# Kernel tuning notes

Measured on AMD Instinct MI355X. Metric: run time of the kernel, lower is better.

## Reference

```python
import jax, jax.numpy as jnp
import numpy as np

TOL_CONTACT = 0.01  # contact tolerance from signed_dis


def _knn_pair(ref_pts, ref_nrm, q_pts, k):
    """Signed distance from each query point to the surface of one other object.

    ref_pts/ref_nrm: [Nr,3] reference object points (in plane frame) and normals.
    q_pts: [Nq,3] query object points (in plane frame). Returns [Nq].
    """
    # brute-force squared distances [Nq, Nr] (same math as tra.nearest_neighbor)
    sq = (jnp.sum(q_pts * q_pts, -1)[:, None]
          - 2.0 * (q_pts @ ref_pts.T)
          + jnp.sum(ref_pts * ref_pts, -1)[None, :])
    negd, idx = jax.lax.top_k(-sq, k)                  # k nearest per query: [Nq,k]
    dist = jnp.sqrt(jnp.maximum(-negd, 0.0))           # euclidean distances
    near = ref_pts[idx]                                # [Nq,k,3] gathered surface pts
    near_n = ref_nrm[idx]                              # [Nq,k,3] gathered normals
    grad = near - q_pts[:, None, :]
    grad = grad / jnp.linalg.norm(grad, axis=-1, keepdims=True)
    insides = jnp.sum(near_n * grad, axis=-1) > 0      # einsum('okij,okij->oki')
    inside = jnp.sum(insides, axis=-1) > k * 0.8       # majority vote over k
    # nearest-neighbor distance, sign-flipped when inside
    return jnp.where(inside, -dist[:, 0], dist[:, 0])


def reference(points, est_T, plane_T, k):
    M, N, _ = points.shape
    # transform object points into plane frame
    T = jnp.linalg.inv(plane_T)[None] @ est_T          # [M,4,4]
    xyz = points[..., :3]
    nrm = points[..., 3:6]
    pts_pl = jnp.einsum('mij,mnj->mni', T[:, :3, :3], xyz) + T[:, None, :3, 3]
    sd_plane = pts_pl[..., 2]                          # plane signed distance [M,N]

    # signed distance of object b's points to every other object o: pair[b,o,:]
    pair = jax.vmap(
        lambda q: jax.vmap(lambda rp, rn: _knn_pair(rp, rn, q, k))(pts_pl, nrm)
    )(pts_pl)                                          # [M,M,N]
    big = jnp.asarray(jnp.finfo(pair.dtype).max, pair.dtype)
    pair = jnp.where(jnp.eye(M, dtype=bool)[:, :, None], big, pair)
    sd_obj = jnp.min(pair, axis=1)                     # min over other objects [M,N]

    signed_distance = jnp.minimum(sd_plane, sd_obj)
    intersects = signed_distance < -TOL_CONTACT
    return signed_distance, intersects


def setup_inputs() -> dict:
    key = jax.random.key(0)
    kp, kn, kt, kpl = jax.random.split(key, 4)
    M, N = 4, 3072
    # objects offset from each other so pairwise nearest distances are > 0
    xyz = jax.random.normal(kp, (M, N, 3), jnp.float32) * 0.05 \
        + jnp.arange(M, dtype=jnp.float32)[:, None, None] * 0.3
    nrm = jax.random.normal(kn, (M, N, 3), jnp.float32)
    nrm = nrm / jnp.linalg.norm(nrm, axis=-1, keepdims=True)
    points = jnp.concatenate([xyz, nrm], axis=-1)      # [M,N,6]

    def rigid(k_, n):
        q, _ = jnp.linalg.qr(jax.random.normal(k_, (n, 3, 3), jnp.float32))
        t = jax.random.normal(jax.random.fold_in(k_, 7), (n, 3), jnp.float32) * 0.1
        T = jnp.zeros((n, 4, 4), jnp.float32)
        T = T.at[:, :3, :3].set(q).at[:, :3, 3].set(t).at[:, 3, 3].set(1.0)
        return T

    est_T = rigid(kt, M)        # per-object estimated transforms [M,4,4]
    plane_T = rigid(kpl, 1)[0]  # plane transform [4,4]
    return {"points": points, "est_T": est_T, "plane_T": plane_T, "k": 10}
```

## Files before the change

### kernel.cpp

```cpp
#include <hip/hip_runtime.h>
#include <math.h>

#define M_OBJ 4
#define N_PTS 3072
#define K_NN  10
#define NSLOT (M_OBJ - 1)
#define QPB   64
#define SEG   4
#define SEGN  (N_PTS / SEG)
#define NCHUNK (SEGN / 64)
#define WSTRIDE 16
#define NWARM (SEGN / WSTRIDE)
#define IDBITS 12
#define IDMASK ((1u << IDBITS) - 1u)

__device__ inline void make_T(const float* __restrict__ E,
                              const float* __restrict__ P,
                              float T[3][4]) {
    float Pi[3][4];
#pragma unroll
    for (int i = 0; i < 3; ++i) {
#pragma unroll
        for (int j = 0; j < 3; ++j) Pi[i][j] = P[j * 4 + i];
        Pi[i][3] = -(P[0 * 4 + i] * P[3] + P[1 * 4 + i] * P[7] + P[2 * 4 + i] * P[11]);
    }
#pragma unroll
    for (int i = 0; i < 3; ++i) {
#pragma unroll
        for (int j = 0; j < 4; ++j) {
            float acc = (j == 3) ? Pi[i][3] : 0.0f;
#pragma unroll
            for (int kk = 0; kk < 3; ++kk) acc += Pi[i][kk] * E[kk * 4 + j];
            T[i][j] = acc;
        }
    }
}

__device__ __forceinline__ void insertv(float v, float bs[K_NN]) {
#pragma unroll
    for (int i = 0; i < K_NN - 1; ++i)
        bs[i] = __builtin_amdgcn_fmed3f(v, bs[i], bs[i + 1]);
    bs[K_NN - 1] = fmaxf(v, bs[K_NN - 1]);
}

__device__ __forceinline__ float score4(const float4 p, float qx, float qy, float qz) {
    return fmaf(p.x, qx, fmaf(p.y, qy, fmaf(p.z, qz, -p.w)));
}

__global__ __launch_bounds__(256, 3) void pair_kernel(
        const float* __restrict__ points,
        const float* __restrict__ estT,
        const float* __restrict__ planeT,
        float* __restrict__ pair_sd) {
    __shared__ float4 sref[N_PTS];
    __shared__ float  mbuf[128 * K_NN];

    const int pidx  = blockIdx.x;
    const int q     = pidx / NSLOT;
    const int rs    = pidx % NSLOT;
    const int r     = rs + (rs >= q ? 1 : 0);
    const int tid   = threadIdx.x;
    const int seg   = tid >> 6;
    const int qlane = tid & 63;

    float Tq[3][4], Tr[3][4];
    make_T(estT + q * 16, planeT, Tq);
    make_T(estT + r * 16, planeT, Tr);

    for (int j = tid; j < N_PTS; j += 256) {
        const float* p = points + (size_t)(r * N_PTS + j) * 6;
        float2 xy = *(const float2*)p;
        float  z  = p[2];
        float px = Tr[0][0] * xy.x + Tr[0][1] * xy.y + Tr[0][2] * z + Tr[0][3];
        float py = Tr[1][0] * xy.x + Tr[1][1] * xy.y + Tr[1][2] * z + Tr[1][3];
        float pz = Tr[2][0] * xy.x + Tr[2][1] * xy.y + Tr[2][2] * z + Tr[2][3];
        float w  = 0.5f * (px * px + py * py + pz * pz);
        sref[j] = make_float4(px, py, pz, w);
    }
    __syncthreads();

    const int nq = blockIdx.y * QPB + qlane;
    const float* qp = points + (size_t)(q * N_PTS + nq) * 6;
    float2 qxy = *(const float2*)qp;
    float  qzz = qp[2];
    const float qx = Tq[0][0] * qxy.x + Tq[0][1] * qxy.y + Tq[0][2] * qzz + Tq[0][3];
    const float qy = Tq[1][0] * qxy.x + Tq[1][1] * qxy.y + Tq[1][2] * qzz + Tq[1][3];
    const float qz = Tq[2][0] * qxy.x + Tq[2][1] * qxy.y + Tq[2][2] * qzz + Tq[2][3];
    const float qq = qx * qx + qy * qy + qz * qz;

    auto pack = [&](int id) -> float {
        float s = score4(sref[id], qx, qy, qz);
        return __uint_as_float((__float_as_uint(s) & ~IDMASK) | (unsigned)id);
    };

    float bs[K_NN];
#pragma unroll
    for (int i = 0; i < K_NN; ++i) bs[i] = -3.4e38f;

    const int j0 = seg * SEGN;

#pragma unroll 4
    for (int t = 0; t < NWARM; ++t)
        insertv(pack(j0 + t * WSTRIDE), bs);

    for (int c = 0; c < NCHUNK; ++c) {
        const int jj = j0 + c * 64;
        const float b0 = bs[0];
        const float gate = fmaf(-fabsf(b0), 1.0e-3f, b0) - 1e-30f;
        unsigned w0 = 0u, w1 = 0u;
#pragma unroll
        for (int b = 0; b < 32; ++b) {
            float s = score4(sref[jj + b], qx, qy, qz);
            w0 |= (s > gate) ? (1u << b) : 0u;
        }
#pragma unroll
        for (int b = 0; b < 32; ++b) {
            float s = score4(sref[jj + 32 + b], qx, qy, qz);
            w1 |= (s > gate) ? (1u << b) : 0u;
        }
        w0 &= ~0x00010001u;
        w1 &= ~0x00010001u;

        while (__any((w0 | w1) != 0u)) {
            if (w0) {
                const int b = __builtin_ctz(w0); w0 &= w0 - 1u;
                insertv(pack(jj + b), bs);
            }
            if (w1) {
                const int b = __builtin_ctz(w1); w1 &= w1 - 1u;
                insertv(pack(jj + 32 + b), bs);
            }
        }
    }

    __syncthreads();
    if (seg >= 2) {
        const int slot = tid - 128;
#pragma unroll
        for (int i = 0; i < K_NN; ++i) mbuf[slot * K_NN + i] = bs[i];
    }
    __syncthreads();
    if (seg < 2) {
        const int src = (seg * 64 + qlane) * K_NN;
#pragma unroll
        for (int i = 0; i < K_NN; ++i) insertv(mbuf[src + i], bs);
    }
    __syncthreads();
    if (seg == 1) {
#pragma unroll
        for (int i = 0; i < K_NN; ++i) mbuf[qlane * K_NN + i] = bs[i];
    }
    __syncthreads();
    if (seg == 0) {
        const int src = qlane * K_NN;
#pragma unroll
        for (int i = 0; i < K_NN; ++i) insertv(mbuf[src + i], bs);

        const float* nrm_base = points + (size_t)r * N_PTS * 6 + 3;
        int votes = 0;
        float s_best = -3.4e38f;
#pragma unroll
        for (int i = 0; i < K_NN; ++i) {
            const int id = (int)(__float_as_uint(bs[i]) & IDMASK);
            float4 p = sref[id];
            float s = score4(p, qx, qy, qz);
            if (i == K_NN - 1) s_best = s;
            const float* nb = nrm_base + (size_t)id * 6;
            float gx = p.x - qx, gy = p.y - qy, gz = p.z - qz;
            votes += (fmaf(nb[0], gx, fmaf(nb[1], gy, nb[2] * gz)) > 0.0f) ? 1 : 0;
        }

        float sq = fmaxf(fmaf(-2.0f, s_best, qq), 0.0f);
        float d0 = sqrtf(sq);
        float sd = (votes > 8) ? -d0 : d0;
        pair_sd[((size_t)q * NSLOT + rs) * N_PTS + nq] = sd;
    }
}

__global__ __launch_bounds__(256) void reduce_kernel(
        const float* __restrict__ points,
        const float* __restrict__ estT,
        const float* __restrict__ planeT,
        const float* __restrict__ pair_sd,
        float* __restrict__ out) {
    int i = blockIdx.x * blockDim.x + threadIdx.x;
    if (i >= M_OBJ * N_PTS) return;
    int m = i / N_PTS, n = i % N_PTS;

    float T[3][4];
    make_T(estT + m * 16, planeT, T);
    const float* p = points + (size_t)i * 6;
    float zpl = T[2][0] * p[0] + T[2][1] * p[1] + T[2][2] * p[2] + T[2][3];

    float sd = zpl;
#pragma unroll
    for (int rs = 0; rs < NSLOT; ++rs)
        sd = fminf(sd, pair_sd[((size_t)m * NSLOT + rs) * N_PTS + n]);

    out[i] = sd;
    out[M_OBJ * N_PTS + i] = (sd < -0.01f) ? 1.0f : 0.0f;
}

extern "C" void kernel_launch(void* const* d_in, const int* in_sizes, int n_in,
                              void* d_out, int out_size, void* d_ws, size_t ws_size,
                              hipStream_t stream) {
    const float* points = (const float*)d_in[0];
    const float* estT   = (const float*)d_in[1];
    const float* planeT = (const float*)d_in[2];

    float* pair_sd = (float*)d_ws;

    dim3 gridB(M_OBJ * NSLOT, N_PTS / QPB);
    pair_kernel<<<gridB, 256, 0, stream>>>(points, estT, planeT, pair_sd);

    int total = M_OBJ * N_PTS;
    reduce_kernel<<<(total + 255) / 256, 256, 0, stream>>>(points, estT, planeT,
                                                           pair_sd, (float*)d_out);
}
```

Measured before the change: 119.7 us.

## Process three queries per thread to reuse shared reference loads

Each thread now tracks top-k lists for three query points, sharing each shared-memory reference float4 load across three score computations. The grid's query dimension shrinks threefold and the launch bound drops to two blocks per CU to accommodate the extra registers. This reduces LDS read traffic and the redundant per-block reference staging, but lowers the number of blocks and serialises the three candidate-insertion loops per thread.

```diff
diff --git a/kernel.cpp b/kernel.cpp
--- a/kernel.cpp
+++ b/kernel.cpp
@@ -5,14 +5,13 @@
 #define N_PTS 3072
 #define K_NN  10
 #define NSLOT (M_OBJ - 1)
-#define QPB   64
-#define SEG   4
-#define SEGN  (N_PTS / SEG)
+#define QSL   3
+#define QPB   (64 * QSL)
+#define NQCH  (N_PTS / QPB)
+#define SEGN  (N_PTS / 4)
 #define NCHUNK (SEGN / 64)
-#define WSTRIDE 16
-#define NWARM (SEGN / WSTRIDE)
-#define IDBITS 12
-#define IDMASK ((1u << IDBITS) - 1u)
+#define NWARM (SEGN / 16)
+#define IDMASK 0xFFFu
 
 __device__ inline void make_T(const float* __restrict__ E,
                               const float* __restrict__ P,
@@ -47,15 +46,21 @@
     return fmaf(p.x, qx, fmaf(p.y, qy, fmaf(p.z, qz, -p.w)));
 }
 
-__global__ __launch_bounds__(256, 3) void pair_kernel(
+#define PACKQ(P, LID, QX, QY, QZ) \
+    __uint_as_float((__float_as_uint(score4((P), (QX), (QY), (QZ))) & ~IDMASK) | (unsigned)(LID))
+
+#define GATE_OF(B0) (fmaf(-fabsf(B0), 1.0e-3f, (B0)) - 1e-30f)
+
+__global__ __launch_bounds__(256, 2) void pair_kernel(
         const float* __restrict__ points,
         const float* __restrict__ estT,
         const float* __restrict__ planeT,
         float* __restrict__ pair_sd) {
     __shared__ float4 sref[N_PTS];
-    __shared__ float  mbuf[128 * K_NN];
+    __shared__ float  mbuf[128 * QSL * K_NN];
 
     const int pidx  = blockIdx.x;
+    const int qc    = blockIdx.y;
     const int q     = pidx / NSLOT;
     const int rs    = pidx % NSLOT;
     const int r     = rs + (rs >= q ? 1 : 0);
@@ -74,62 +79,87 @@
         float px = Tr[0][0] * xy.x + Tr[0][1] * xy.y + Tr[0][2] * z + Tr[0][3];
         float py = Tr[1][0] * xy.x + Tr[1][1] * xy.y + Tr[1][2] * z + Tr[1][3];
         float pz = Tr[2][0] * xy.x + Tr[2][1] * xy.y + Tr[2][2] * z + Tr[2][3];
-        float w  = 0.5f * (px * px + py * py + pz * pz);
-        sref[j] = make_float4(px, py, pz, w);
-    }
-    __syncthreads();
-
-    const int nq = blockIdx.y * QPB + qlane;
-    const float* qp = points + (size_t)(q * N_PTS + nq) * 6;
-    float2 qxy = *(const float2*)qp;
-    float  qzz = qp[2];
-    const float qx = Tq[0][0] * qxy.x + Tq[0][1] * qxy.y + Tq[0][2] * qzz + Tq[0][3];
-    const float qy = Tq[1][0] * qxy.x + Tq[1][1] * qxy.y + Tq[1][2] * qzz + Tq[1][3];
-    const float qz = Tq[2][0] * qxy.x + Tq[2][1] * qxy.y + Tq[2][2] * qzz + Tq[2][3];
-    const float qq = qx * qx + qy * qy + qz * qz;
-
-    auto pack = [&](int id) -> float {
-        float s = score4(sref[id], qx, qy, qz);
-        return __uint_as_float((__float_as_uint(s) & ~IDMASK) | (unsigned)id);
-    };
-
-    float bs[K_NN];
-#pragma unroll
-    for (int i = 0; i < K_NN; ++i) bs[i] = -3.4e38f;
+        sref[j] = make_float4(px, py, pz, 0.5f * (px * px + py * py + pz * pz));
+    }
+    __syncthreads();
+
+    const int nqA = qc * QPB + 0 * 64 + qlane;
+    const int nqB = qc * QPB + 1 * 64 + qlane;
+    const int nqC = qc * QPB + 2 * 64 + qlane;
+    const float* qpA = points + (size_t)(q * N_PTS + nqA) * 6;
+    const float* qpB = points + (size_t)(q * N_PTS + nqB) * 6;
+    const float* qpC = points + (size_t)(q * N_PTS + nqC) * 6;
+    float2 axy = *(const float2*)qpA; float az = qpA[2];
+    float2 bxy = *(const float2*)qpB; float bz = qpB[2];
+    float2 cxy = *(const float2*)qpC; float cz = qpC[2];
+    const float qxA = Tq[0][0]*axy.x + Tq[0][1]*axy.y + Tq[0][2]*az + Tq[0][3];
+    const float qyA = Tq[1][0]*axy.x + Tq[1][1]*axy.y + Tq[1][2]*az + Tq[1][3];
+    const float qzA = Tq[2][0]*axy.x + Tq[2][1]*axy.y + Tq[2][2]*az + Tq[2][3];
+    const float qxB = Tq[0][0]*bxy.x + Tq[0][1]*bxy.y + Tq[0][2]*bz + Tq[0][3];
+    const float qyB = Tq[1][0]*bxy.x + Tq[1][1]*bxy.y + Tq[1][2]*bz + Tq[1][3];
+    const float qzB = Tq[2][0]*bxy.x + Tq[2][1]*bxy.y + Tq[2][2]*bz + Tq[2][3];
+    const float qxC = Tq[0][0]*cxy.x + Tq[0][1]*cxy.y + Tq[0][2]*cz + Tq[0][3];
+    const float qyC = Tq[1][0]*cxy.x + Tq[1][1]*cxy.y + Tq[1][2]*cz + Tq[1][3];
+    const float qzC = Tq[2][0]*cxy.x + Tq[2][1]*cxy.y + Tq[2][2]*cz + Tq[2][3];
+    const float qqA = qxA*qxA + qyA*qyA + qzA*qzA;
+    const float qqB = qxB*qxB + qyB*qyB + qzB*qzB;
+    const float qqC = qxC*qxC + qyC*qyC + qzC*qzC;
+
+    float bsA[K_NN], bsB[K_NN], bsC[K_NN];
+#pragma unroll
+    for (int i = 0; i < K_NN; ++i) { bsA[i] = -3.4e38f; bsB[i] = -3.4e38f; bsC[i] = -3.4e38f; }
 
     const int j0 = seg * SEGN;
 
-#pragma unroll 4
-    for (int t = 0; t < NWARM; ++t)
-        insertv(pack(j0 + t * WSTRIDE), bs);
+    for (int k = 0; k < NWARM; ++k) {
+        const int lid = j0 + k * 16;
+        const float4 p = sref[lid];
+        insertv(PACKQ(p, lid, qxA, qyA, qzA), bsA);
+        insertv(PACKQ(p, lid, qxB, qyB, qzB), bsB);
+        insertv(PACKQ(p, lid, qxC, qyC, qzC), bsC);
+    }
 
     for (int c = 0; c < NCHUNK; ++c) {
         const int jj = j0 + c * 64;
-        const float b0 = bs[0];
-        const float gate = fmaf(-fabsf(b0), 1.0e-3f, b0) - 1e-30f;
-        unsigned w0 = 0u, w1 = 0u;
+        const float gA = GATE_OF(bsA[0]);
+        const float gB = GATE_OF(bsB[0]);
+        const float gC = GATE_OF(bsC[0]);
+        unsigned mA0 = 0u, mA1 = 0u, mB0 = 0u, mB1 = 0u, mC0 = 0u, mC1 = 0u;
 #pragma unroll
         for (int b = 0; b < 32; ++b) {
-            float s = score4(sref[jj + b], qx, qy, qz);
-            w0 |= (s > gate) ? (1u << b) : 0u;
+            const float4 p = sref[jj + b];
+            mA0 |= (score4(p, qxA, qyA, qzA) > gA) ? (1u << b) : 0u;
+            mB0 |= (score4(p, qxB, qyB, qzB) > gB) ? (1u << b) : 0u;
+            mC0 |= (score4(p, qxC, qyC, qzC) > gC) ? (1u << b) : 0u;
         }
 #pragma unroll
         for (int b = 0; b < 32; ++b) {
-            float s = score4(sref[jj + 32 + b], qx, qy, qz);
-            w1 |= (s > gate) ? (1u << b) : 0u;
-        }
-        w0 &= ~0x00010001u;
-        w1 &= ~0x00010001u;
-
-        while (__any((w0 | w1) != 0u)) {
-            if (w0) {
-                const int b = __builtin_ctz(w0); w0 &= w0 - 1u;
-                insertv(pack(jj + b), bs);
-            }
-            if (w1) {
-                const int b = __builtin_ctz(w1); w1 &= w1 - 1u;
-                insertv(pack(jj + 32 + b), bs);
-            }
+            const float4 p = sref[jj + 32 + b];
+            mA1 |= (score4(p, qxA, qyA, qzA) > gA) ? (1u << b) : 0u;
+            mB1 |= (score4(p, qxB, qyB, qzB) > gB) ? (1u << b) : 0u;
+            mC1 |= (score4(p, qxC, qyC, qzC) > gC) ? (1u << b) : 0u;
+        }
+        mA0 &= ~0x00010001u; mA1 &= ~0x00010001u;
+        mB0 &= ~0x00010001u; mB1 &= ~0x00010001u;
+        mC0 &= ~0x00010001u; mC1 &= ~0x00010001u;
+
+        while (__any((mA0 | mA1) != 0u)) {
+            if (mA0) { const int b = __builtin_ctz(mA0); mA0 &= mA0 - 1u;
+                const int lid = jj + b;      insertv(PACKQ(sref[lid], lid, qxA, qyA, qzA), bsA); }
+            if (mA1) { const int b = __builtin_ctz(mA1); mA1 &= mA1 - 1u;
+                const int lid = jj + 32 + b; insertv(PACKQ(sref[lid], lid, qxA, qyA, qzA), bsA); }
+        }
+        while (__any((mB0 | mB1) != 0u)) {
+            if (mB0) { const int b = __builtin_ctz(mB0); mB0 &= mB0 - 1u;
+                const int lid = jj + b;      insertv(PACKQ(sref[lid], lid, qxB, qyB, qzB), bsB); }
+            if (mB1) { const int b = __builtin_ctz(mB1); mB1 &= mB1 - 1u;
+                const int lid = jj + 32 + b; insertv(PACKQ(sref[lid], lid, qxB, qyB, qzB), bsB); }
+        }
+        while (__any((mC0 | mC1) != 0u)) {
+            if (mC0) { const int b = __builtin_ctz(mC0); mC0 &= mC0 - 1u;
+                const int lid = jj + b;      insertv(PACKQ(sref[lid], lid, qxC, qyC, qzC), bsC); }
+            if (mC1) { const int b = __builtin_ctz(mC1); mC1 &= mC1 - 1u;
+                const int lid = jj + 32 + b; insertv(PACKQ(sref[lid], lid, qxC, qyC, qzC), bsC); }
         }
     }
 
@@ -137,43 +167,84 @@
     if (seg >= 2) {
         const int slot = tid - 128;
 #pragma unroll
-        for (int i = 0; i < K_NN; ++i) mbuf[slot * K_NN + i] = bs[i];
+        for (int i = 0; i < K_NN; ++i) {
+            mbuf[(slot * QSL + 0) * K_NN + i] = bsA[i];
+            mbuf[(slot * QSL + 1) * K_NN + i] = bsB[i];
+            mbuf[(slot * QSL + 2) * K_NN + i] = bsC[i];
+        }
     }
     __syncthreads();
     if (seg < 2) {
-        const int src = (seg * 64 + qlane) * K_NN;
-#pragma unroll
-        for (int i = 0; i < K_NN; ++i) insertv(mbuf[src + i], bs);
+        const int src = seg * 64 + qlane;
+#pragma unroll
+        for (int i = 0; i < K_NN; ++i) {
+            insertv(mbuf[(src * QSL + 0) * K_NN + i], bsA);
+            insertv(mbuf[(src * QSL + 1) * K_NN + i], bsB);
+            insertv(mbuf[(src * QSL + 2) * K_NN + i], bsC);
+        }
     }
     __syncthreads();
     if (seg == 1) {
 #pragma unroll
-        for (int i = 0; i < K_NN; ++i) mbuf[qlane * K_NN + i] = bs[i];
+        for (int i = 0; i < K_NN; ++i) {
+            mbuf[(qlane * QSL + 0) * K_NN + i] = bsA[i];
+            mbuf[(qlane * QSL + 1) * K_NN + i] = bsB[i];
+            mbuf[(qlane * QSL + 2) * K_NN + i] = bsC[i];
+        }
     }
     __syncthreads();
     if (seg == 0) {
-        const int src = qlane * K_NN;
-#pragma unroll
-        for (int i = 0; i < K_NN; ++i) insertv(mbuf[src + i], bs);
+#pragma unroll
+        for (int i = 0; i < K_NN; ++i) {
+            insertv(mbuf[(qlane * QSL + 0) * K_NN + i], bsA);
+            insertv(mbuf[(qlane * QSL + 1) * K_NN + i], bsB);
+            insertv(mbuf[(qlane * QSL + 2) * K_NN + i], bsC);
+        }
 
         const float* nrm_base = points + (size_t)r * N_PTS * 6 + 3;
-        int votes = 0;
-        float s_best = -3.4e38f;
-#pragma unroll
-        for (int i = 0; i < K_NN; ++i) {
-            const int id = (int)(__float_as_uint(bs[i]) & IDMASK);
-            float4 p = sref[id];
-            float s = score4(p, qx, qy, qz);
-            if (i == K_NN - 1) s_best = s;
-            const float* nb = nrm_base + (size_t)id * 6;
-            float gx = p.x - qx, gy = p.y - qy, gz = p.z - qz;
-            votes += (fmaf(nb[0], gx, fmaf(nb[1], gy, nb[2] * gz)) > 0.0f) ? 1 : 0;
-        }
-
-        float sq = fmaxf(fmaf(-2.0f, s_best, qq), 0.0f);
-        float d0 = sqrtf(sq);
-        float sd = (votes > 8) ? -d0 : d0;
-        pair_sd[((size_t)q * NSLOT + rs) * N_PTS + nq] = sd;
+
+        {
+            int votes = 0; float s_best = -3.4e38f;
+#pragma unroll
+            for (int i = 0; i < K_NN; ++i) {
+                const int id = (int)(__float_as_uint(bsA[i]) & IDMASK);
+                const float4 p = sref[id];
+                const float s = score4(p, qxA, qyA, qzA);
+                if (i == K_NN - 1) s_best = s;
+                const float* nb = nrm_base + (size_t)id * 6;
+                votes += (fmaf(nb[0], p.x-qxA, fmaf(nb[1], p.y-qyA, nb[2]*(p.z-qzA))) > 0.0f) ? 1 : 0;
+            }
+            const float d0 = sqrtf(fmaxf(fmaf(-2.0f, s_best, qqA), 0.0f));
+            pair_sd[((size_t)q * NSLOT + rs) * N_PTS + nqA] = (votes > 8) ? -d0 : d0;
+        }
+        {
+            int votes = 0; float s_best = -3.4e38f;
+#pragma unroll
+            for (int i = 0; i < K_NN; ++i) {
+                const int id = (int)(__float_as_uint(bsB[i]) & IDMASK);
+                const float4 p = sref[id];
+                const float s = score4(p, qxB, qyB, qzB);
+                if (i == K_NN - 1) s_best = s;
+                const float* nb = nrm_base + (size_t)id * 6;
+                votes += (fmaf(nb[0], p.x-qxB, fmaf(nb[1], p.y-qyB, nb[2]*(p.z-qzB))) > 0.0f) ? 1 : 0;
+            }
+            const float d0 = sqrtf(fmaxf(fmaf(-2.0f, s_best, qqB), 0.0f));
+            pair_sd[((size_t)q * NSLOT + rs) * N_PTS + nqB] = (votes > 8) ? -d0 : d0;
+        }
+        {
+            int votes = 0; float s_best = -3.4e38f;
+#pragma unroll
+            for (int i = 0; i < K_NN; ++i) {
+                const int id = (int)(__float_as_uint(bsC[i]) & IDMASK);
+                const float4 p = sref[id];
+                const float s = score4(p, qxC, qyC, qzC);
+                if (i == K_NN - 1) s_best = s;
+                const float* nb = nrm_base + (size_t)id * 6;
+                votes += (fmaf(nb[0], p.x-qxC, fmaf(nb[1], p.y-qyC, nb[2]*(p.z-qzC))) > 0.0f) ? 1 : 0;
+            }
+            const float d0 = sqrtf(fmaxf(fmaf(-2.0f, s_best, qqC), 0.0f));
+            pair_sd[((size_t)q * NSLOT + rs) * N_PTS + nqC] = (votes > 8) ? -d0 : d0;
+        }
     }
 }
 
@@ -190,9 +261,7 @@
     float T[3][4];
     make_T(estT + m * 16, planeT, T);
     const float* p = points + (size_t)i * 6;
-    float zpl = T[2][0] * p[0] + T[2][1] * p[1] + T[2][2] * p[2] + T[2][3];
-
-    float sd = zpl;
+    float sd = T[2][0]*p[0] + T[2][1]*p[1] + T[2][2]*p[2] + T[2][3];
 #pragma unroll
     for (int rs = 0; rs < NSLOT; ++rs)
         sd = fminf(sd, pair_sd[((size_t)m * NSLOT + rs) * N_PTS + n]);
@@ -210,7 +279,7 @@
 
     float* pair_sd = (float*)d_ws;
 
-    dim3 gridB(M_OBJ * NSLOT, N_PTS / QPB);
+    dim3 gridB(M_OBJ * NSLOT, NQCH);
     pair_kernel<<<gridB, 256, 0, stream>>>(points, estT, planeT, pair_sd);
 
     int total = M_OBJ * N_PTS;
```

After: 348.2 us. 191% more time.

## Share top-k pruning threshold across segment warps and widen scan chunks

Applied to the files above, without the earlier changes.

After the strided warm-up pass, each of the four segment warps writes its current k-th-best score to shared memory. Every warp then gates candidates against the maximum of those four values, and refreshes it once mid-scan. This prunes more insertion work than using only the warp's own running k-th best. The scan loop also tests 128 reference points per iteration with four bitmasks instead of 64, which amortises the divergent insertion loop. The cost is extra block barriers and a larger register footprint under the 3-blocks-per-SM launch bound.

```diff
diff --git a/kernel.cpp b/kernel.cpp
--- a/kernel.cpp
+++ b/kernel.cpp
@@ -6,13 +6,10 @@
 #define K_NN  10
 #define NSLOT (M_OBJ - 1)
 #define QPB   64
-#define SEG   4
-#define SEGN  (N_PTS / SEG)
+#define SEGN  (N_PTS / 4)
 #define NCHUNK (SEGN / 64)
-#define WSTRIDE 16
-#define NWARM (SEGN / WSTRIDE)
-#define IDBITS 12
-#define IDMASK ((1u << IDBITS) - 1u)
+#define NWARM (SEGN / 16)
+#define IDMASK 0xFFFu
 
 __device__ inline void make_T(const float* __restrict__ E,
                               const float* __restrict__ P,
@@ -46,6 +43,10 @@
 __device__ __forceinline__ float score4(const float4 p, float qx, float qy, float qz) {
     return fmaf(p.x, qx, fmaf(p.y, qy, fmaf(p.z, qz, -p.w)));
 }
+
+#define PACKQ(P, LID, QX, QY, QZ) \
+    __uint_as_float((__float_as_uint(score4((P), (QX), (QY), (QZ))) & ~IDMASK) | (unsigned)(LID))
+#define GATE_OF(B0) (fmaf(-fabsf(B0), 1.0e-3f, (B0)) - 1e-30f)
 
 __global__ __launch_bounds__(256, 3) void pair_kernel(
         const float* __restrict__ points,
@@ -74,8 +75,7 @@
         float px = Tr[0][0] * xy.x + Tr[0][1] * xy.y + Tr[0][2] * z + Tr[0][3];
         float py = Tr[1][0] * xy.x + Tr[1][1] * xy.y + Tr[1][2] * z + Tr[1][3];
         float pz = Tr[2][0] * xy.x + Tr[2][1] * xy.y + Tr[2][2] * z + Tr[2][3];
-        float w  = 0.5f * (px * px + py * py + pz * pz);
-        sref[j] = make_float4(px, py, pz, w);
+        sref[j] = make_float4(px, py, pz, 0.5f * (px * px + py * py + pz * pz));
     }
     __syncthreads();
 
@@ -83,15 +83,10 @@
     const float* qp = points + (size_t)(q * N_PTS + nq) * 6;
     float2 qxy = *(const float2*)qp;
     float  qzz = qp[2];
-    const float qx = Tq[0][0] * qxy.x + Tq[0][1] * qxy.y + Tq[0][2] * qzz + Tq[0][3];
-    const float qy = Tq[1][0] * qxy.x + Tq[1][1] * qxy.y + Tq[1][2] * qzz + Tq[1][3];
-    const float qz = Tq[2][0] * qxy.x + Tq[2][1] * qxy.y + Tq[2][2] * qzz + Tq[2][3];
-    const float qq = qx * qx + qy * qy + qz * qz;
-
-    auto pack = [&](int id) -> float {
-        float s = score4(sref[id], qx, qy, qz);
-        return __uint_as_float((__float_as_uint(s) & ~IDMASK) | (unsigned)id);
-    };
+    const float qx = Tq[0][0]*qxy.x + Tq[0][1]*qxy.y + Tq[0][2]*qzz + Tq[0][3];
+    const float qy = Tq[1][0]*qxy.x + Tq[1][1]*qxy.y + Tq[1][2]*qzz + Tq[1][3];
+    const float qz = Tq[2][0]*qxy.x + Tq[2][1]*qxy.y + Tq[2][2]*qzz + Tq[2][3];
+    const float qq = qx*qx + qy*qy + qz*qz;
 
     float bs[K_NN];
 #pragma unroll
@@ -100,36 +95,59 @@
     const int j0 = seg * SEGN;
 
 #pragma unroll 4
-    for (int t = 0; t < NWARM; ++t)
-        insertv(pack(j0 + t * WSTRIDE), bs);
-
-    for (int c = 0; c < NCHUNK; ++c) {
+    for (int t = 0; t < NWARM; ++t) {
+        const int lid = j0 + t * 16;
+        insertv(PACKQ(sref[lid], lid, qx, qy, qz), bs);
+    }
+
+    mbuf[seg * 64 + qlane] = bs[0];
+    __syncthreads();
+    float sthr = fmaxf(fmaxf(mbuf[qlane], mbuf[64 + qlane]),
+                       fmaxf(mbuf[128 + qlane], mbuf[192 + qlane]));
+
+    for (int c = 0; c < NCHUNK; c += 2) {
+        if (c == 6) {
+            __syncthreads();
+            mbuf[seg * 64 + qlane] = bs[0];
+            __syncthreads();
+            sthr = fmaxf(fmaxf(mbuf[qlane], mbuf[64 + qlane]),
+                         fmaxf(mbuf[128 + qlane], mbuf[192 + qlane]));
+        }
         const int jj = j0 + c * 64;
-        const float b0 = bs[0];
-        const float gate = fmaf(-fabsf(b0), 1.0e-3f, b0) - 1e-30f;
-        unsigned w0 = 0u, w1 = 0u;
+        const float g = GATE_OF(fmaxf(bs[0], sthr));
+        unsigned u0 = 0u, u1 = 0u, v0 = 0u, v1 = 0u;
 #pragma unroll
         for (int b = 0; b < 32; ++b) {
             float s = score4(sref[jj + b], qx, qy, qz);
-            w0 |= (s > gate) ? (1u << b) : 0u;
+            u0 |= (s > g) ? (1u << b) : 0u;
         }
 #pragma unroll
         for (int b = 0; b < 32; ++b) {
             float s = score4(sref[jj + 32 + b], qx, qy, qz);
-            w1 |= (s > gate) ? (1u << b) : 0u;
-        }
-        w0 &= ~0x00010001u;
-        w1 &= ~0x00010001u;
-
-        while (__any((w0 | w1) != 0u)) {
-            if (w0) {
-                const int b = __builtin_ctz(w0); w0 &= w0 - 1u;
-                insertv(pack(jj + b), bs);
-            }
-            if (w1) {
-                const int b = __builtin_ctz(w1); w1 &= w1 - 1u;
-                insertv(pack(jj + 32 + b), bs);
-            }
+            u1 |= (s > g) ? (1u << b) : 0u;
+        }
+#pragma unroll
+        for (int b = 0; b < 32; ++b) {
+            float s = score4(sref[jj + 64 + b], qx, qy, qz);
+            v0 |= (s > g) ? (1u << b) : 0u;
+        }
+#pragma unroll
+        for (int b = 0; b < 32; ++b) {
+            float s = score4(sref[jj + 96 + b], qx, qy, qz);
+            v1 |= (s > g) ? (1u << b) : 0u;
+        }
+        u0 &= ~0x00010001u; u1 &= ~0x00010001u;
+        v0 &= ~0x00010001u; v1 &= ~0x00010001u;
+
+        while (__any((u0 | u1 | v0 | v1) != 0u)) {
+            if (u0) { const int b = __builtin_ctz(u0); u0 &= u0 - 1u;
+                const int lid = jj + b;      insertv(PACKQ(sref[lid], lid, qx, qy, qz), bs); }
+            if (u1) { const int b = __builtin_ctz(u1); u1 &= u1 - 1u;
+                const int lid = jj + 32 + b; insertv(PACKQ(sref[lid], lid, qx, qy, qz), bs); }
+            if (v0) { const int b = __builtin_ctz(v0); v0 &= v0 - 1u;
+                const int lid = jj + 64 + b; insertv(PACKQ(sref[lid], lid, qx, qy, qz), bs); }
+            if (v1) { const int b = __builtin_ctz(v1); v1 &= v1 - 1u;
+                const int lid = jj + 96 + b; insertv(PACKQ(sref[lid], lid, qx, qy, qz), bs); }
         }
     }
 
@@ -162,18 +180,15 @@
 #pragma unroll
         for (int i = 0; i < K_NN; ++i) {
             const int id = (int)(__float_as_uint(bs[i]) & IDMASK);
-            float4 p = sref[id];
-            float s = score4(p, qx, qy, qz);
+            const float4 p = sref[id];
+            const float s = score4(p, qx, qy, qz);
             if (i == K_NN - 1) s_best = s;
             const float* nb = nrm_base + (size_t)id * 6;
-            float gx = p.x - qx, gy = p.y - qy, gz = p.z - qz;
-            votes += (fmaf(nb[0], gx, fmaf(nb[1], gy, nb[2] * gz)) > 0.0f) ? 1 : 0;
-        }
-
-        float sq = fmaxf(fmaf(-2.0f, s_best, qq), 0.0f);
-        float d0 = sqrtf(sq);
-        float sd = (votes > 8) ? -d0 : d0;
-        pair_sd[((size_t)q * NSLOT + rs) * N_PTS + nq] = sd;
+            votes += (fmaf(nb[0], p.x-qx, fmaf(nb[1], p.y-qy, nb[2]*(p.z-qz))) > 0.0f) ? 1 : 0;
+        }
+
+        const float d0 = sqrtf(fmaxf(fmaf(-2.0f, s_best, qq), 0.0f));
+        pair_sd[((size_t)q * NSLOT + rs) * N_PTS + nq] = (votes > 8) ? -d0 : d0;
     }
 }
 
@@ -190,9 +205,7 @@
     float T[3][4];
     make_T(estT + m * 16, planeT, T);
     const float* p = points + (size_t)i * 6;
-    float zpl = T[2][0] * p[0] + T[2][1] * p[1] + T[2][2] * p[2] + T[2][3];
-
-    float sd = zpl;
+    float sd = T[2][0]*p[0] + T[2][1]*p[1] + T[2][2]*p[2] + T[2][3];
 #pragma unroll
     for (int rs = 0; rs < NSLOT; ++rs)
         sd = fminf(sd, pair_sd[((size_t)m * NSLOT + rs) * N_PTS + n]);
```

Result: slower. 123.8 us (+3.4%).
